# Kernel tuning notes

Measured on AMD Instinct MI355X. Metric: run time of the kernel, lower is better.

Reference implementation:

```python
import jax, jax.numpy as jnp
import numpy as np

STATE_DIM = 256
ACT_LEN = 16
LATENT = 256
ENC = 512
SLOPE = 0.01  # torch.nn.LeakyReLU() default


def _leaky(x):
    return jnp.where(x >= 0, x, SLOPE * x)


def setup_inputs() -> dict:
    key = jax.random.key(0)
    ks = jax.random.split(key, 16)
    B, T = 64, 1024
    D = STATE_DIM + 2 * ACT_LEN
    s = lambda k, shp, fan_in: jax.random.normal(k, shp, dtype=jnp.float32) * (1.0 / np.sqrt(fan_in))
    return {
        "padded_input": jax.random.normal(ks[0], (B, T, D), dtype=jnp.float32),
        # encoder: Linear(state,enc)+leaky, Linear(enc,enc)+leaky, Linear(enc,latent)+leaky
        "enc_w1": s(ks[1], (STATE_DIM, ENC), STATE_DIM), "enc_b1": jnp.zeros((ENC,), jnp.float32),
        "enc_w2": s(ks[2], (ENC, ENC), ENC),             "enc_b2": jnp.zeros((ENC,), jnp.float32),
        "enc_w3": s(ks[3], (ENC, LATENT), ENC),          "enc_b3": jnp.zeros((LATENT,), jnp.float32),
        # latent dynamics (bias-free)
        "A_w": s(ks[4], (LATENT, LATENT), LATENT),
        "B_w": s(ks[5], (ACT_LEN, LATENT), ACT_LEN),
        # decoder: Linear(latent,enc)+leaky, Linear(enc,enc)+leaky, Linear(enc,state)
        "dec_w1": s(ks[6], (LATENT, ENC), LATENT),       "dec_b1": jnp.zeros((ENC,), jnp.float32),
        "dec_w2": s(ks[7], (ENC, ENC), ENC),             "dec_b2": jnp.zeros((ENC,), jnp.float32),
        "dec_w3": s(ks[8], (ENC, STATE_DIM), ENC),       "dec_b3": jnp.zeros((STATE_DIM,), jnp.float32),
    }


def reference(padded_input, enc_w1, enc_b1, enc_w2, enc_b2, enc_w3, enc_b3,
              A_w, B_w, dec_w1, dec_b1, dec_w2, dec_b2, dec_w3, dec_b3):
    # slice features: [state | u_t | u_t1]
    x_t = padded_input[:, :, :STATE_DIM]                       # [B,T,S]
    u_t1 = padded_input[:, :, STATE_DIM + ACT_LEN:]            # [B,T,A]

    # encoder MLP
    h = _leaky(x_t @ enc_w1 + enc_b1)
    h = _leaky(h @ enc_w2 + enc_b2)
    z_t = _leaky(h @ enc_w3 + enc_b3)                          # [B,T,L]

    # reset_probability=0, nwarmup=0: t=0 uses z_t[:,0], then pure recurrence
    # z1[t] = A z1[t-1] + B u_t1[t]
    Bu = u_t1 @ B_w                                            # [B,T,L]

    def step(prev, bu_t):
        new = prev @ A_w + bu_t                                # [B,L]
        return new, new

    _, z1 = jax.lax.scan(step, z_t[:, 0, :], jnp.swapaxes(Bu, 0, 1))
    z_t1 = jnp.swapaxes(z1, 0, 1)                              # [B,T,L]

    # decoder MLP (last layer linear)
    h = _leaky(z_t1 @ dec_w1 + dec_b1)
    h = _leaky(h @ dec_w2 + dec_b2)
    x_t1 = h @ dec_w3 + dec_b3                                 # [B,T,S]
    return x_t1
```

## Files before the change

### kernel.cpp

```cpp
#include <hip/hip_runtime.h>

constexpr int Bb  = 64;
constexpr int Tt  = 1024;
constexpr int Dd  = 288;
constexpr int Ss  = 256;
constexpr int ALa = 16;
constexpr int Ll  = 256;
constexpr int Ee  = 512;
constexpr int CC  = 8;
constexpr int NCh = 128;
constexpr int NSC = 16;
constexpr int SC  = 8;
constexpr int DEC_CHUNKS = 8;
constexpr int DEC_ROWS = (Bb*Tt)/DEC_CHUNKS;

#define LKY(v) ((v) >= 0.f ? (v) : 0.01f*(v))

using f32x4  = __attribute__((ext_vector_type(4))) float;
using short8 = __attribute__((ext_vector_type(8))) short;
typedef unsigned short ushort_t;

__device__ __forceinline__ unsigned short f2bf(float f){
  unsigned int u = __float_as_uint(f);
  u = (u + 0x7fffu + ((u >> 16) & 1u)) >> 16;
  return (unsigned short)u;
}
__device__ __forceinline__ float bf2f(unsigned short h){
  return __uint_as_float(((unsigned int)h) << 16);
}

__global__ __launch_bounds__(256) void enc_fused(
    const float* __restrict__ in0,
    const float* __restrict__ w1, const float* __restrict__ b1,
    const float* __restrict__ w2, const float* __restrict__ b2,
    const float* __restrict__ w3, const float* __restrict__ b3,
    float* __restrict__ z0)
{
  int b = blockIdx.x, tid = threadIdx.x;
  __shared__ float xb[512], h1[512];
  xb[tid] = (tid < 256) ? in0[(long)b*(Tt*Dd) + tid] : 0.f;
  __syncthreads();
  float a0 = b1[tid], a1 = b1[tid+256];
  #pragma unroll 4
  for (int k = 0; k < 256; ++k){
    float xv = xb[k];
    a0 = fmaf(xv, w1[k*512 + tid      ], a0);
    a1 = fmaf(xv, w1[k*512 + tid + 256], a1);
  }
  __syncthreads();
  h1[tid] = LKY(a0); h1[tid+256] = LKY(a1);
  __syncthreads();
  float c0 = b2[tid], c1 = b2[tid+256];
  #pragma unroll 4
  for (int k = 0; k < 512; ++k){
    float hv = h1[k];
    c0 = fmaf(hv, w2[k*512 + tid      ], c0);
    c1 = fmaf(hv, w2[k*512 + tid + 256], c1);
  }
  __syncthreads();
  xb[tid] = LKY(c0); xb[tid+256] = LKY(c1);
  __syncthreads();
  float d0 = b3[tid];
  #pragma unroll 4
  for (int k = 0; k < 512; ++k)
    d0 = fmaf(xb[k], w3[k*256 + tid], d0);
  z0[b*256 + tid] = LKY(d0);
}

struct MMJob { const float* X; const float* Y; float* Cf; ushort_t* Ch; ushort_t* Cl; };
struct MMJobs { MMJob j[4]; };

__global__ __launch_bounds__(256) void matmul_gb(MMJobs jobs)
{
  MMJob jb = jobs.j[blockIdx.y];
  int i = blockIdx.x;
  int tid = threadIdx.x;
  int jg = tid & 63, tk = tid >> 6;
  __shared__ float row[256];
  __shared__ float4 part[4][64];
  if (tid < 256) row[tid] = jb.X[i*256 + tid];
  __syncthreads();
  int j4 = jg*4;
  float4 p0 = make_float4(0,0,0,0), p1 = make_float4(0,0,0,0);
  int kb = tk*64;
  #pragma unroll 4
  for (int k = kb; k < kb+64; k += 2){
    float x0 = row[k], x1 = row[k+1];
    float4 y0 = *(const float4*)&jb.Y[(k  )*256 + j4];
    float4 y1 = *(const float4*)&jb.Y[(k+1)*256 + j4];
    p0.x = fmaf(x0,y0.x,p0.x); p0.y = fmaf(x0,y0.y,p0.y);
    p0.z = fmaf(x0,y0.z,p0.z); p0.w = fmaf(x0,y0.w,p0.w);
    p1.x = fmaf(x1,y1.x,p1.x); p1.y = fmaf(x1,y1.y,p1.y);
    p1.z = fmaf(x1,y1.z,p1.z); p1.w = fmaf(x1,y1.w,p1.w);
  }
  p0.x+=p1.x; p0.y+=p1.y; p0.z+=p1.z; p0.w+=p1.w;
  part[tk][jg] = p0;
  __syncthreads();
  if (tid < 64){
    float4 s = part[0][tid];
    #pragma unroll
    for (int q = 1; q < 4; ++q){
      float4 v = part[q][tid];
      s.x+=v.x; s.y+=v.y; s.z+=v.z; s.w+=v.w;
    }
    int j = tid*4;
    if (jb.Cf) *(float4*)&jb.Cf[i*256 + j] = s;
    if (jb.Ch){
      float vv[4] = {s.x,s.y,s.z,s.w};
      #pragma unroll
      for (int e = 0; e < 4; ++e){
        ushort_t h = f2bf(vv[e]);
        int o = ((i>>3)*256 + j + e)*8 + (i&7);
        jb.Ch[o] = h; jb.Cl[o] = f2bf(vv[e] - bf2f(h));
      }
    }
  }
}

__global__ __launch_bounds__(256) void prep_a1bw(
    const float* __restrict__ A, const float* __restrict__ B,
    ushort_t* __restrict__ AH, ushort_t* __restrict__ AL,
    ushort_t* __restrict__ Bh, ushort_t* __restrict__ Bl)
{
  int o = blockIdx.x*256 + threadIdx.x;
  if (o < 65536){
    int j = o & 7, rest = o >> 3;
    int n = rest & 255, t8 = rest >> 8;
    int k = t8*8 + j;
    float v = A[k*256 + n];
    ushort_t h = f2bf(v);
    AH[o] = h; AL[o] = f2bf(v - bf2f(h));
  } else {
    int ob = o - 65536;
    int j = ob & 7, rest = ob >> 3;
    int n = rest & 255, kq = rest >> 8;
    int k = kq*8 + j;
    float v = (k < ALa) ? B[k*256 + n] : 0.f;
    ushort_t h = f2bf(v);
    Bh[ob] = h; Bl[ob] = f2bf(v - bf2f(h));
  }
}

__global__ __launch_bounds__(256) void prep_dec(
    const float* __restrict__ w1, const float* __restrict__ w2,
    const float* __restrict__ w3, ushort_t* __restrict__ Wh,
    ushort_t* __restrict__ Wl)
{
  long o = (long)blockIdx.x*256 + threadIdx.x;
  const float* W; ushort_t* H; ushort_t* L; int N; long oo;
  if (o < 131072){ W = w1; H = Wh;          L = Wl;          N = 512; oo = o; }
  else if (o < 393216){ W = w2; H = Wh + 131072; L = Wl + 131072; N = 512; oo = o - 131072; }
  else { W = w3; H = Wh + 393216; L = Wl + 393216; N = 256; oo = o - 393216; }
  int j = (int)(oo & 7);
  long rest = oo >> 3;
  int n = (int)(rest % N);
  int t8 = (int)(rest / N);
  int k = t8*8 + j;
  float v = W[(long)k*N + n];
  ushort_t h = f2bf(v);
  H[oo] = h; L[oo] = f2bf(v - bf2f(h));
}

__device__ __forceinline__ void load_afrag(
    const ushort_t* __restrict__ P, int kq, int m0, short8* dst)
{
  #pragma unroll
  for (int mt = 0; mt < 4; ++mt)
    dst[mt] = *(const short8*)&P[((long)kq*256 + m0 + mt*16)*8];
}

__global__ __launch_bounds__(256) void scan_mfma(
    const float* __restrict__ in0,
    const ushort_t* __restrict__ AtH, const ushort_t* __restrict__ AtL,
    const ushort_t* __restrict__ BtH, const ushort_t* __restrict__ BtL,
    float* __restrict__ wend, float* __restrict__ zout)
{
  int chunk = blockIdx.x;
  int n0 = blockIdx.y * 32;
  int tid = threadIdx.x;
  int wave = tid >> 6, lane = tid & 63;
  int quad = lane >> 4, l16 = lane & 15;
  int mwave = wave * 64;
  int m0 = mwave + l16;

  __shared__ ushort_t StH[8192];
  __shared__ ushort_t StL[8192];

  short8 Bfh[4], Bfl[4];
  #pragma unroll
  for (int mt = 0; mt < 4; ++mt){
    int off = ((quad)*256 + m0 + mt*16)*8;
    Bfh[mt] = *(const short8*)&BtH[off];
    Bfl[mt] = *(const short8*)&BtL[off];
  }

  f32x4 acc[4][2];
  #pragma unroll
  for (int mt = 0; mt < 4; ++mt)
    #pragma unroll
    for (int nt = 0; nt < 2; ++nt) acc[mt][nt] = (f32x4){0.f,0.f,0.f,0.f};

  const float* ubase[2];
  #pragma unroll
  for (int nt = 0; nt < 2; ++nt)
    ubase[nt] = in0 + (long)(n0 + nt*16 + l16)*(Tt*Dd) + (Ss + ALa) + quad*8;

  short8 Ahb[2][4], Alb[2][4];

  for (int tt = 0; tt < CC; ++tt){
    int t = chunk*CC + tt;
    float4 uq[2][2];
    #pragma unroll
    for (int nt = 0; nt < 2; ++nt){
      if (quad < 2){
        const float* up = ubase[nt] + (long)t*Dd;
        uq[nt][0] = *(const float4*)up;
        uq[nt][1] = *(const float4*)(up + 4);
      } else {
        uq[nt][0] = make_float4(0,0,0,0); uq[nt][1] = make_float4(0,0,0,0);
      }
    }

    if (tt > 0){
      load_afrag(AtH, 0*4 + quad, m0, Ahb[0]);
      load_afrag(AtL, 0*4 + quad, m0, Alb[0]);
      #pragma unroll
      for (int kt = 0; kt < 8; ++kt){
        int cur = kt & 1;
        if (kt < 7){
          load_afrag(AtH, (kt+1)*4 + quad, m0, Ahb[cur^1]);
          load_afrag(AtL, (kt+1)*4 + quad, m0, Alb[cur^1]);
        }
        short8 Sbh[2], Sbl[2];
        #pragma unroll
        for (int nt = 0; nt < 2; ++nt){
          int off = ((kt*4 + quad)*32 + nt*16 + l16)*8;
          Sbh[nt] = *(const short8*)&StH[off];
          Sbl[nt] = *(const short8*)&StL[off];
        }
        #pragma unroll
        for (int mt = 0; mt < 4; ++mt)
          #pragma unroll
          for (int nt = 0; nt < 2; ++nt){
            acc[mt][nt] = __builtin_amdgcn_mfma_f32_16x16x32_bf16(Ahb[cur][mt], Sbh[nt], acc[mt][nt], 0,0,0);
            acc[mt][nt] = __builtin_amdgcn_mfma_f32_16x16x32_bf16(Ahb[cur][mt], Sbl[nt], acc[mt][nt], 0,0,0);
            acc[mt][nt] = __builtin_amdgcn_mfma_f32_16x16x32_bf16(Alb[cur][mt], Sbh[nt], acc[mt][nt], 0,0,0);
          }
      }
    }

    short8 uh[2], ul[2];
    #pragma unroll
    for (int nt = 0; nt < 2; ++nt){
      float v[8] = {uq[nt][0].x,uq[nt][0].y,uq[nt][0].z,uq[nt][0].w,
                    uq[nt][1].x,uq[nt][1].y,uq[nt][1].z,uq[nt][1].w};
      ushort_t hs[8], ls[8];
      #pragma unroll
      for (int j = 0; j < 8; ++j){
        hs[j] = f2bf(v[j]);
        ls[j] = f2bf(v[j] - bf2f(hs[j]));
      }
      uh[nt] = *(const short8*)hs; ul[nt] = *(const short8*)ls;
    }
    #pragma unroll
    for (int mt = 0; mt < 4; ++mt)
      #pragma unroll
      for (int nt = 0; nt < 2; ++nt){
        acc[mt][nt] = __builtin_amdgcn_mfma_f32_16x16x32_bf16(Bfh[mt], uh[nt], acc[mt][nt], 0,0,0);
        acc[mt][nt] = __builtin_amdgcn_mfma_f32_16x16x32_bf16(Bfh[mt], ul[nt], acc[mt][nt], 0,0,0);
        acc[mt][nt] = __builtin_amdgcn_mfma_f32_16x16x32_bf16(Bfl[mt], uh[nt], acc[mt][nt], 0,0,0);
      }

    __syncthreads();

    #pragma unroll
    for (int mt = 0; mt < 4; ++mt){
      int mb = mwave + mt*16 + quad*4;
      #pragma unroll
      for (int nt = 0; nt < 2; ++nt){
        int n = nt*16 + l16;
        int gn = n0 + n;
        f32x4 v = acc[mt][nt];
        *(float4*)&zout[((long)gn*Tt + t)*Ll + mb] = make_float4(v[0],v[1],v[2],v[3]);
        if (tt == CC-1)
          *(float4*)&wend[((long)chunk*Bb + gn)*Ll + mb] = make_float4(v[0],v[1],v[2],v[3]);
        #pragma unroll
        for (int reg = 0; reg < 4; ++reg){
          int m = mb + reg;
          ushort_t h = f2bf(v[reg]);
          ushort_t l = f2bf(v[reg] - bf2f(h));
          int so = ((m>>3)*32 + n)*8 + (m&7);
          StH[so] = h; StL[so] = l;
        }
        acc[mt][nt] = (f32x4){0.f,0.f,0.f,0.f};
      }
    }
    __syncthreads();
  }
}

__device__ __forceinline__ void frag_init_state512(
    const float* __restrict__ src, ushort_t* StH, ushort_t* StL, int tid)
{
  #pragma unroll
  for (int it = 0; it < 4; ++it){
    int idx = tid + it*512;
    int m8 = idx >> 6, n = idx & 63;
    const float* p = src + (long)n*256 + m8*8;
    float4 v0 = *(const float4*)p;
    float4 v1 = *(const float4*)(p + 4);
    float vv[8] = {v0.x,v0.y,v0.z,v0.w,v1.x,v1.y,v1.z,v1.w};
    ushort_t hs[8], ls[8];
    #pragma unroll
    for (int j = 0; j < 8; ++j){
      hs[j] = f2bf(vv[j]);
      ls[j] = f2bf(vv[j] - bf2f(hs[j]));
    }
    *(uint4*)&StH[(m8*64 + n)*8] = *(const uint4*)hs;
    *(uint4*)&StL[(m8*64 + n)*8] = *(const uint4*)ls;
  }
}

__device__ __forceinline__ void p2_load_A(
    const ushort_t* __restrict__ PH, const ushort_t* __restrict__ PL,
    int wave, int lane, short8 Ah[2][8], short8 Al[2][8])
{
  int quad = lane >> 4, l16 = lane & 15;
  int m0 = wave*32 + l16;
  #pragma unroll
  for (int kt = 0; kt < 8; ++kt){
    int kq = kt*4 + quad;
    #pragma unroll
    for (int mt = 0; mt < 2; ++mt){
      Ah[mt][kt] = *(const short8*)&PH[((long)kq*256 + m0 + mt*16)*8];
      Al[mt][kt] = *(const short8*)&PL[((long)kq*256 + m0 + mt*16)*8];
    }
  }
}

__device__ __forceinline__ void ks_gemm_body(
    const ushort_t* __restrict__ PH, const ushort_t* __restrict__ PL,
    const float* __restrict__ accsrc, const float* __restrict__ bsrc,
    float* __restrict__ outp, ushort_t* StH, ushort_t* StL)
{
  int tid = threadIdx.x;
  int wave = tid >> 6, lane = tid & 63;
  int quad = lane >> 4, l16 = lane & 15;
  int mwave = wave*32;

  short8 Ah[2][8], Al[2][8];
  p2_load_A(PH, PL, wave, lane, Ah, Al);
  frag_init_state512(bsrc, StH, StL, tid);

  f32x4 acc[2][4];
  #pragma unroll
  for (int mt = 0; mt < 2; ++mt){
    int mb = mwave + mt*16 + quad*4;
    #pragma unroll
    for (int nt = 0; nt < 4; ++nt){
      int n = nt*16 + l16;
      float4 v = *(const float4*)&accsrc[(long)n*256 + mb];
      acc[mt][nt] = (f32x4){v.x, v.y, v.z, v.w};
    }
  }
  __syncthreads();

  #pragma unroll
  for (int kt = 0; kt < 8; ++kt){
    #pragma unroll
    for (int nt = 0; nt < 4; ++nt){
      int off = ((kt*4 + quad)*64 + nt*16 + l16)*8;
      short8 Sbh = *(const short8*)&StH[off];
      short8 Sbl = *(const short8*)&StL[off];
      #pragma unroll
      for (int mt = 0; mt < 2; ++mt){
        acc[mt][nt] = __builtin_amdgcn_mfma_f32_16x16x32_bf16(Ah[mt][kt], Sbh, acc[mt][nt], 0,0,0);
        acc[mt][nt] = __builtin_amdgcn_mfma_f32_16x16x32_bf16(Ah[mt][kt], Sbl, acc[mt][nt], 0,0,0);
        acc[mt][nt] = __builtin_amdgcn_mfma_f32_16x16x32_bf16(Al[mt][kt], Sbh, acc[mt][nt], 0,0,0);
      }
    }
  }

  #pragma unroll
  for (int mt = 0; mt < 2; ++mt){
    int mb = mwave + mt*16 + quad*4;
    #pragma unroll
    for (int nt = 0; nt < 4; ++nt){
      int n = nt*16 + l16;
      f32x4 v = acc[mt][nt];
      *(float4*)&outp[(long)n*256 + mb] = make_float4(v[0],v[1],v[2],v[3]);
    }
  }
}

__device__ __forceinline__ const float* ks_src(
    const float* __restrict__ in, const float* __restrict__ z0,
    const float* __restrict__ pbend, int c, int init_mode)
{
  if (!init_mode) return in + (long)c*(Bb*Ll);
  return (c == 0) ? z0 : (pbend + (long)(8*c - 1)*(Bb*Ll));
}

__global__ __launch_bounds__(512) void ks_round(
    const ushort_t* __restrict__ PH, const ushort_t* __restrict__ PL,
    const float* __restrict__ in, const float* __restrict__ z0,
    const float* __restrict__ pbend,
    float* __restrict__ out, long outStride, int d, int local_seg, int init_mode)
{
  int c = blockIdx.x;
  int tid = threadIdx.x;
  int pos = local_seg ? (c & 7) : c;
  const float* src_c = ks_src(in, z0, pbend, c, init_mode);
  float* op = out + (long)c*outStride;

  if (pos < d){
    const float4* s4p = (const float4*)src_c;
    float4* d4p = (float4*)op;
    #pragma unroll
    for (int it = 0; it < 8; ++it) d4p[tid + it*512] = s4p[tid + it*512];
    return;
  }
  const float* src_cd = ks_src(in, z0, pbend, c - d, init_mode);
  __shared__ ushort_t StH[16384], StL[16384];
  ks_gemm_body(PH, PL, src_c, src_cd, op, StH, StL);
}

__global__ __launch_bounds__(512) void replay_corr(
    const ushort_t* __restrict__ A8H, const ushort_t* __restrict__ A8L,
    const ushort_t* __restrict__ A8PH, const ushort_t* __restrict__ A8PL,
    const float* __restrict__ pb, float* __restrict__ inits)
{
  int i = blockIdx.x + 1;
  int s = blockIdx.y;
  const ushort_t* PH = (i == 1) ? A8H : (A8PH + (long)(i-1)*65536);
  const ushort_t* PL = (i == 1) ? A8L : (A8PL + (long)(i-1)*65536);
  __shared__ ushort_t StH[16384], StL[16384];
  ks_gemm_body(PH, PL,
               pb + (long)(8*s + i - 1)*(Bb*Ll),
               inits + (long)(8*s)*(Bb*Ll),
               inits + (long)(8*s + i)*(Bb*Ll), StH, StL);
}

__global__ __launch_bounds__(256) void gemm_corr(
    const float* __restrict__ inits, const ushort_t* __restrict__ AjH,
    const ushort_t* __restrict__ AjL, float* __restrict__ out)
{
  int jz = blockIdx.z;
  const ushort_t* Whp = AjH + (long)jz*65536;
  const ushort_t* Wlp = AjL + (long)jz*65536;
  __shared__ __align__(16) ushort_t Xh[4*128*8], Xl[4*128*8];
  __shared__ __align__(16) ushort_t Wh[4*128*8], Wl[4*128*8];

  int tid  = threadIdx.x;
  int wave = tid >> 6, lane = tid & 63;
  int wm = wave & 1, wn = wave >> 1;
  int quad = lane >> 4, l16 = lane & 15;
  int row0 = blockIdx.y * 128;
  int col0 = blockIdx.x * 128;

  f32x4 acc[4][4];
  #pragma unroll
  for (int mt = 0; mt < 4; ++mt)
    #pragma unroll
    for (int nt = 0; nt < 4; ++nt) acc[mt][nt] = (f32x4){0.f,0.f,0.f,0.f};

  for (int kt = 0; kt < 8; ++kt){
    #pragma unroll
    for (int it = 0; it < 2; ++it){
      int idx = tid + it*256;
      int q = idx >> 7, m = idx & 127;
      const float* xp = &inits[(long)(row0 + m)*256 + kt*32 + q*8];
      float4 v0 = *(const float4*)xp;
      float4 v1 = *(const float4*)(xp + 4);
      float vv[8] = {v0.x,v0.y,v0.z,v0.w,v1.x,v1.y,v1.z,v1.w};
      ushort_t hs[8], ls[8];
      #pragma unroll
      for (int j = 0; j < 8; ++j){
        hs[j] = f2bf(vv[j]);
        ls[j] = f2bf(vv[j] - bf2f(hs[j]));
      }
      *(uint4*)&Xh[(q*128 + m)*8] = *(const uint4*)hs;
      *(uint4*)&Xl[(q*128 + m)*8] = *(const uint4*)ls;
      int n = idx & 127;
      long src = (long)(kt*4 + q)*256 + col0 + n;
      ((uint4*)Wh)[q*128 + n] = ((const uint4*)Whp)[src];
      ((uint4*)Wl)[q*128 + n] = ((const uint4*)Wlp)[src];
    }
    __syncthreads();
    short8 ah[4], al[4], bh[4], bl[4];
    #pragma unroll
    for (int mt = 0; mt < 4; ++mt){
      int off = (quad*128 + wm*64 + mt*16 + l16)*8;
      ah[mt] = *(const short8*)&Xh[off];
      al[mt] = *(const short8*)&Xl[off];
    }
    #pragma unroll
    for (int nt = 0; nt < 4; ++nt){
      int off = (quad*128 + wn*64 + nt*16 + l16)*8;
      bh[nt] = *(const short8*)&Wh[off];
      bl[nt] = *(const short8*)&Wl[off];
    }
    #pragma unroll
    for (int mt = 0; mt < 4; ++mt)
      #pragma unroll
      for (int nt = 0; nt < 4; ++nt){
        acc[mt][nt] = __builtin_amdgcn_mfma_f32_16x16x32_bf16(ah[mt], bh[nt], acc[mt][nt], 0,0,0);
        acc[mt][nt] = __builtin_amdgcn_mfma_f32_16x16x32_bf16(ah[mt], bl[nt], acc[mt][nt], 0,0,0);
        acc[mt][nt] = __builtin_amdgcn_mfma_f32_16x16x32_bf16(al[mt], bh[nt], acc[mt][nt], 0,0,0);
      }
    __syncthreads();
  }

  #pragma unroll
  for (int mt = 0; mt < 4; ++mt){
    #pragma unroll
    for (int nt = 0; nt < 4; ++nt){
      int col = col0 + wn*64 + nt*16 + l16;
      #pragma unroll
      for (int reg = 0; reg < 4; ++reg){
        int row = row0 + wm*64 + mt*16 + quad*4 + reg;
        int b = row & 63, c = row >> 6;
        int t = c*CC + jz;
        long addr = ((long)b*Tt + t)*Ll + col;
        out[addr] += acc[mt][nt][reg];
      }
    }
  }
}

template<int BM, int BN, bool INS, bool OUTS>
__global__ __launch_bounds__(256) void gemm_mfma(
    const float* __restrict__ X,
    const ushort_t* __restrict__ Xhp, const ushort_t* __restrict__ Xlp,
    const ushort_t* __restrict__ Whp, const ushort_t* __restrict__ Wlp,
    const float* __restrict__ bias, float* __restrict__ Y,
    ushort_t* __restrict__ Yh, ushort_t* __restrict__ Yl,
    int Mrows, int K, int N, int act)
{
  constexpr int BMh = BM/2, BNh = BN/2;
  constexpr int MT = BM/32, NT = BN/32;
  __shared__ __align__(16) ushort_t Xh[4*BM*8], Xl[4*BM*8];
  __shared__ __align__(16) ushort_t Wh[4*BN*8], Wl[4*BN*8];

  int tid  = threadIdx.x;
  int wave = tid >> 6, lane = tid & 63;
  int wm = wave & 1, wn = wave >> 1;
  int quad = lane >> 4, l16 = lane & 15;
  long row0 = (long)blockIdx.y * BM;
  int col0 = blockIdx.x * BN;

  f32x4 acc[MT][NT];
  #pragma unroll
  for (int mt = 0; mt < MT; ++mt)
    #pragma unroll
    for (int nt = 0; nt < NT; ++nt) acc[mt][nt] = (f32x4){0.f,0.f,0.f,0.f};

  for (int kt = 0; kt < K; kt += 32){
    int ktile = kt >> 5;
    if constexpr (INS){
      #pragma unroll
      for (int it = 0; it < (BM*4)/256; ++it){
        int idx = tid + it*256;
        int q = idx / BM, m = idx % BM;
        long src = (long)(ktile*4 + q)*Mrows + row0 + m;
        ((uint4*)Xh)[q*BM + m] = ((const uint4*)Xhp)[src];
        ((uint4*)Xl)[q*BM + m] = ((const uint4*)Xlp)[src];
      }
    } else {
      #pragma unroll
      for (int it = 0; it < (BM*4)/256; ++it){
        int idx = tid + it*256;
        int q = idx / BM, m = idx % BM;
        const float* xp = &X[(row0 + m)*(long)K + kt + q*8];
        float4 v0 = *(const float4*)xp;
        float4 v1 = *(const float4*)(xp + 4);
        float vv[8] = {v0.x,v0.y,v0.z,v0.w,v1.x,v1.y,v1.z,v1.w};
        ushort_t hs[8], ls[8];
        #pragma unroll
        for (int j = 0; j < 8; ++j){
          hs[j] = f2bf(vv[j]);
          ls[j] = f2bf(vv[j] - bf2f(hs[j]));
        }
        *(uint4*)&Xh[(q*BM + m)*8] = *(const uint4*)hs;
        *(uint4*)&Xl[(q*BM + m)*8] = *(const uint4*)ls;
      }
    }
    #pragma unroll
    for (int it = 0; it < (BN*4)/256; ++it){
      int idx = tid + it*256;
      int q = idx / BN, n = idx % BN;
      long src = (long)(ktile*4 + q)*N + col0 + n;
      ((uint4*)Wh)[q*BN + n] = ((const uint4*)Whp)[src];
      ((uint4*)Wl)[q*BN + n] = ((const uint4*)Wlp)[src];
    }
    __syncthreads();

    short8 ah[MT], al[MT], bh[NT], bl[NT];
    #pragma unroll
    for (int mt = 0; mt < MT; ++mt){
      int off = (quad*BM + wm*BMh + mt*16 + l16)*8;
      ah[mt] = *(const short8*)&Xh[off];
      al[mt] = *(const short8*)&Xl[off];
    }
    #pragma unroll
    for (int nt = 0; nt < NT; ++nt){
      int off = (quad*BN + wn*BNh + nt*16 + l16)*8;
      bh[nt] = *(const short8*)&Wh[off];
      bl[nt] = *(const short8*)&Wl[off];
    }
    #pragma unroll
    for (int mt = 0; mt < MT; ++mt)
      #pragma unroll
      for (int nt = 0; nt < NT; ++nt){
        acc[mt][nt] = __builtin_amdgcn_mfma_f32_16x16x32_bf16(ah[mt], bh[nt], acc[mt][nt], 0, 0, 0);
        acc[mt][nt] = __builtin_amdgcn_mfma_f32_16x16x32_bf16(ah[mt], bl[nt], acc[mt][nt], 0, 0, 0);
        acc[mt][nt] = __builtin_amdgcn_mfma_f32_16x16x32_bf16(al[mt], bh[nt], acc[mt][nt], 0, 0, 0);
      }
    __syncthreads();
  }

  #pragma unroll
  for (int mt = 0; mt < MT; ++mt){
    long rowb = row0 + wm*BMh + mt*16 + quad*4;
    #pragma unroll
    for (int nt = 0; nt < NT; ++nt){
      int col = col0 + wn*BNh + nt*16 + l16;
      float bs = bias[col];
      #pragma unroll
      for (int reg = 0; reg < 4; ++reg){
        float y = acc[mt][nt][reg] + bs;
        if (act) y = LKY(y);
        long row = rowb + reg;
        if constexpr (OUTS){
          ushort_t h = f2bf(y);
          ushort_t l = f2bf(y - bf2f(h));
          long off = ((long)(col >> 3)*Mrows + row)*8 + (col & 7);
          Yh[off] = h; Yl[off] = l;
        } else {
          Y[row*(long)N + col] = y;
        }
      }
    }
  }
}

extern "C" void kernel_launch(void* const* d_in, const int* in_sizes, int n_in,
                              void* d_out, int out_size, void* d_ws, size_t ws_size,
                              hipStream_t stream) {
  const float* in0    = (const float*)d_in[0];
  const float* enc_w1 = (const float*)d_in[1];
  const float* enc_b1 = (const float*)d_in[2];
  const float* enc_w2 = (const float*)d_in[3];
  const float* enc_b2 = (const float*)d_in[4];
  const float* enc_w3 = (const float*)d_in[5];
  const float* enc_b3 = (const float*)d_in[6];
  const float* A_w    = (const float*)d_in[7];
  const float* B_w    = (const float*)d_in[8];
  const float* dec_w1 = (const float*)d_in[9];
  const float* dec_b1 = (const float*)d_in[10];
  const float* dec_w2 = (const float*)d_in[11];
  const float* dec_b2 = (const float*)d_in[12];
  const float* dec_w3 = (const float*)d_in[13];
  const float* dec_b3 = (const float*)d_in[14];
  float* out = (float*)d_out;

  float* ws    = (float*)d_ws;
  float* s2    = ws + 65536;
  float* s3    = ws + 131072;
  float* s4    = ws + 196608;
  float* s8    = ws + 262144;
  float* s16   = ws + 327680;
  float* s32   = ws + 393216;
  float* s64   = ws + 458752;
  ushort_t* Whp_d = (ushort_t*)(ws + 524288);
  ushort_t* Wlp_d = (ushort_t*)(ws + 786432);
  float* Rf    = ws + 1048576;
  ushort_t* AjH = (ushort_t*)Rf;
  ushort_t* AjL = (ushort_t*)(Rf + 262144);
  ushort_t* BtH = (ushort_t*)(Rf + 524288);
  ushort_t* BtL = BtH + 8192;
  float* wend  = Rf + 532480;
  float* inits = Rf + 2629632;
  float* g0    = Rf + 4726784;
  ushort_t* A64H = (ushort_t*)(Rf + 4988928);
  ushort_t* A64L = (ushort_t*)(Rf + 5021696);
  float* pb0   = Rf + 5054464;
  ushort_t* A8PH = (ushort_t*)(Rf + 7151616);
  ushort_t* A8PL = (ushort_t*)(Rf + 7380992);
  ushort_t* A64PH = (ushort_t*)(Rf + 7610368);
  ushort_t* A64PL = (ushort_t*)(Rf + 7708672);
  float* f24   = Rf + 7806976;
  float* f128  = Rf + 7872512;
  float* f256  = Rf + 7938048;
  float* g1    = Rf + 8003584;
  ushort_t* h1h = (ushort_t*)Rf;
  ushort_t* h1l = (ushort_t*)(Rf + 2097152);
  ushort_t* h2h = (ushort_t*)(Rf + 4194304);
  ushort_t* h2l = (ushort_t*)(Rf + 6291456);
  ushort_t* A8H = AjH + 7*65536;
  ushort_t* A8L = AjL + 7*65536;

  enc_fused<<<64, 256, 0, stream>>>(in0, enc_w1, enc_b1, enc_w2, enc_b2,
                                    enc_w3, enc_b3, inits);

  prep_a1bw<<<288, 256, 0, stream>>>(A_w, B_w, AjH, AjL, BtH, BtL);

  auto mj = [](const float* X, const float* Y, float* Cf, ushort_t* Ch, ushort_t* Cl){
    MMJob r; r.X = X; r.Y = Y; r.Cf = Cf; r.Ch = Ch; r.Cl = Cl; return r;
  };
  { MMJobs J = {};
    J.j[0] = mj(A_w, A_w, s2, AjH+1*65536, AjL+1*65536);
    matmul_gb<<<dim3(256,1), 256, 0, stream>>>(J); }
  { MMJobs J = {};
    J.j[0] = mj(s2, A_w, s3, AjH+2*65536, AjL+2*65536);
    J.j[1] = mj(s2, s2,  s4, AjH+3*65536, AjL+3*65536);
    matmul_gb<<<dim3(256,2), 256, 0, stream>>>(J); }
  { MMJobs J = {};
    J.j[0] = mj(s4, A_w, nullptr, AjH+4*65536, AjL+4*65536);
    J.j[1] = mj(s4, s2,  nullptr, AjH+5*65536, AjL+5*65536);
    J.j[2] = mj(s4, s3,  nullptr, AjH+6*65536, AjL+6*65536);
    J.j[3] = mj(s4, s4,  s8, A8H, A8L);
    matmul_gb<<<dim3(256,4), 256, 0, stream>>>(J); }
  { MMJobs J = {};
    J.j[0] = mj(s8, s8, s16, A8PH+1*65536, A8PL+1*65536);
    matmul_gb<<<dim3(256,1), 256, 0, stream>>>(J); }
  { MMJobs J = {};
    J.j[0] = mj(s16, s8,  f24, A8PH+2*65536, A8PL+2*65536);
    J.j[1] = mj(s16, s16, s32, A8PH+3*65536, A8PL+3*65536);
    matmul_gb<<<dim3(256,2), 256, 0, stream>>>(J); }
  { MMJobs J = {};
    J.j[0] = mj(s32, s8,  nullptr, A8PH+4*65536, A8PL+4*65536);
    J.j[1] = mj(s32, s16, nullptr, A8PH+5*65536, A8PL+5*65536);
    J.j[2] = mj(s32, f24, nullptr, A8PH+6*65536, A8PL+6*65536);
    J.j[3] = mj(s32, s32, s64, A64H, A64L);
    matmul_gb<<<dim3(256,4), 256, 0, stream>>>(J); }
  { MMJobs J = {};
    J.j[0] = mj(s64, s64, f128, A64PH+0*65536, A64PL+0*65536);
    matmul_gb<<<dim3(256,1), 256, 0, stream>>>(J); }
  { MMJobs J = {};
    J.j[0] = mj(f128, f128, f256, A64PH+1*65536, A64PL+1*65536);
    matmul_gb<<<dim3(256,1), 256, 0, stream>>>(J); }
  { MMJobs J = {};
    J.j[0] = mj(f256, f256, nullptr, A64PH+2*65536, A64PL+2*65536);
    matmul_gb<<<dim3(256,1), 256, 0, stream>>>(J); }

  prep_dec<<<2048, 256, 0, stream>>>(dec_w1, dec_w2, dec_w3, Whp_d, Wlp_d);

  scan_mfma<<<dim3(NCh, 2), 256, 0, stream>>>(in0, AjH, AjL, BtH, BtL, wend, out);

  ks_round<<<128, 512, 0, stream>>>(A8H, A8L, wend, nullptr, nullptr, pb0, Bb*Ll, 1, 1, 0);
  ks_round<<<128, 512, 0, stream>>>(A8PH+1*65536, A8PL+1*65536, pb0, nullptr, nullptr, wend, Bb*Ll, 2, 1, 0);
  ks_round<<<128, 512, 0, stream>>>(A8PH+3*65536, A8PL+3*65536, wend, nullptr, nullptr, pb0, Bb*Ll, 4, 1, 0);
  ks_round<<<16, 512, 0, stream>>>(A64H, A64L, nullptr, inits, pb0, g1, Bb*Ll, 1, 0, 1);
  ks_round<<<16, 512, 0, stream>>>(A64PH+0*65536, A64PL+0*65536, g1, nullptr, nullptr, g0, Bb*Ll, 2, 0, 0);
  ks_round<<<16, 512, 0, stream>>>(A64PH+1*65536, A64PL+1*65536, g0, nullptr, nullptr, g1, Bb*Ll, 4, 0, 0);
  ks_round<<<16, 512, 0, stream>>>(A64PH+2*65536, A64PL+2*65536, g1, nullptr, nullptr, inits, (long)SC*Bb*Ll, 8, 0, 0);
  replay_corr<<<dim3(7, 16), 512, 0, stream>>>(A8H, A8L, A8PH, A8PL, pb0, inits);

  gemm_corr<<<dim3(2, 64, 8), 256, 0, stream>>>(inits, AjH, AjL, out);

  for (int rc = 0; rc < DEC_CHUNKS; ++rc){
    const float* zc = out + (long)rc*DEC_ROWS*Ll;
    float* oc       = out + (long)rc*DEC_ROWS*Ll;
    gemm_mfma<64,128,false,true><<<dim3(Ee/128, DEC_ROWS/64), 256, 0, stream>>>(
        zc, nullptr, nullptr, Whp_d, Wlp_d, dec_b1, nullptr, h1h, h1l, DEC_ROWS, Ll, Ee, 1);
    gemm_mfma<64,128,true,true><<<dim3(Ee/128, DEC_ROWS/64), 256, 0, stream>>>(
        nullptr, h1h, h1l, Whp_d + 131072, Wlp_d + 131072, dec_b2, nullptr, h2h, h2l, DEC_ROWS, Ee, Ee, 1);
    gemm_mfma<64,128,true,false><<<dim3(Ss/128, DEC_ROWS/64), 256, 0, stream>>>(
        nullptr, h2h, h2l, Whp_d + 393216, Wlp_d + 393216, dec_b3, oc, nullptr, nullptr, DEC_ROWS, Ee, Ss, 0);
  }
}
```

Before: 1.021 ms.

## Split encoder into parallel dense layer kernels and enlarge decoder GEMM tiles

The single-block-per-batch fused encoder, which ran only 64 blocks, is replaced by three launches of a generic dense kernel. Each launch is split over output-column tiles with a K-split shared-memory reduction, so many more blocks run in parallel. Intermediate activations now go through workspace memory, which adds launches and global traffic. Separately, the first two decoder GEMMs use 128-row tiles instead of 64, which halves the grid size and raises weight reuse per block.

```diff
diff --git a/kernel.cpp b/kernel.cpp
--- a/kernel.cpp
+++ b/kernel.cpp
@@ -29,42 +29,38 @@
   return __uint_as_float(((unsigned int)h) << 16);
 }
 
-__global__ __launch_bounds__(256) void enc_fused(
-    const float* __restrict__ in0,
-    const float* __restrict__ w1, const float* __restrict__ b1,
-    const float* __restrict__ w2, const float* __restrict__ b2,
-    const float* __restrict__ w3, const float* __restrict__ b3,
-    float* __restrict__ z0)
-{
-  int b = blockIdx.x, tid = threadIdx.x;
-  __shared__ float xb[512], h1[512];
-  xb[tid] = (tid < 256) ? in0[(long)b*(Tt*Dd) + tid] : 0.f;
+__global__ __launch_bounds__(256) void enc_dense(
+    const float* __restrict__ xin, int xstride,
+    const float* __restrict__ W, const float* __restrict__ bias,
+    float* __restrict__ out, int K, int N, int act)
+{
+  int b = blockIdx.x, col0 = blockIdx.y * 32;
+  int tid = threadIdx.x;
+  int tx = tid & 31, tk = tid >> 5;
+  __shared__ float x[512];
+  __shared__ float part[8][33];
+  for (int k = tid; k < K; k += 256) x[k] = xin[(long)b*xstride + k];
   __syncthreads();
-  float a0 = b1[tid], a1 = b1[tid+256];
-  #pragma unroll 4
-  for (int k = 0; k < 256; ++k){
-    float xv = xb[k];
-    a0 = fmaf(xv, w1[k*512 + tid      ], a0);
-    a1 = fmaf(xv, w1[k*512 + tid + 256], a1);
-  }
+  int j = col0 + tx;
+  float p0=0.f,p1=0.f,p2=0.f,p3=0.f;
+  int iters = K >> 3;
+  #pragma unroll 2
+  for (int i = 0; i < iters; i += 4){
+    int k0 = tk + 8*i;
+    p0 = fmaf(x[k0     ], W[(long)(k0     )*N + j], p0);
+    p1 = fmaf(x[k0 +  8], W[(long)(k0 +  8)*N + j], p1);
+    p2 = fmaf(x[k0 + 16], W[(long)(k0 + 16)*N + j], p2);
+    p3 = fmaf(x[k0 + 24], W[(long)(k0 + 24)*N + j], p3);
+  }
+  part[tk][tx] = (p0+p1)+(p2+p3);
   __syncthreads();
-  h1[tid] = LKY(a0); h1[tid+256] = LKY(a1);
-  __syncthreads();
-  float c0 = b2[tid], c1 = b2[tid+256];
-  #pragma unroll 4
-  for (int k = 0; k < 512; ++k){
-    float hv = h1[k];
-    c0 = fmaf(hv, w2[k*512 + tid      ], c0);
-    c1 = fmaf(hv, w2[k*512 + tid + 256], c1);
-  }
-  __syncthreads();
-  xb[tid] = LKY(c0); xb[tid+256] = LKY(c1);
-  __syncthreads();
-  float d0 = b3[tid];
-  #pragma unroll 4
-  for (int k = 0; k < 512; ++k)
-    d0 = fmaf(xb[k], w3[k*256 + tid], d0);
-  z0[b*256 + tid] = LKY(d0);
+  if (tid < 32){
+    float s = part[0][tid];
+    #pragma unroll
+    for (int q = 1; q < 8; ++q) s += part[q][tid];
+    s += bias[col0 + tid];
+    out[b*N + col0 + tid] = act ? LKY(s) : s;
+  }
 }
 
 struct MMJob { const float* X; const float* Y; float* Cf; ushort_t* Ch; ushort_t* Cl; };
@@ -665,6 +661,8 @@
   float* out = (float*)d_out;
 
   float* ws    = (float*)d_ws;
+  float* h1enc = ws;
+  float* h2enc = ws + 32768;
   float* s2    = ws + 65536;
   float* s3    = ws + 131072;
   float* s4    = ws + 196608;
@@ -700,8 +698,9 @@
   ushort_t* A8H = AjH + 7*65536;
   ushort_t* A8L = AjL + 7*65536;
 
-  enc_fused<<<64, 256, 0, stream>>>(in0, enc_w1, enc_b1, enc_w2, enc_b2,
-                                    enc_w3, enc_b3, inits);
+  enc_dense<<<dim3(64,16), 256, 0, stream>>>(in0, Tt*Dd, enc_w1, enc_b1, h1enc, 256, 512, 1);
+  enc_dense<<<dim3(64,16), 256, 0, stream>>>(h1enc, 512, enc_w2, enc_b2, h2enc, 512, 512, 1);
+  enc_dense<<<dim3(64, 8), 256, 0, stream>>>(h2enc, 512, enc_w3, enc_b3, inits, 512, 256, 1);
 
   prep_a1bw<<<288, 256, 0, stream>>>(A_w, B_w, AjH, AjL, BtH, BtL);
 
@@ -762,9 +761,9 @@
   for (int rc = 0; rc < DEC_CHUNKS; ++rc){
     const float* zc = out + (long)rc*DEC_ROWS*Ll;
     float* oc       = out + (long)rc*DEC_ROWS*Ll;
-    gemm_mfma<64,128,false,true><<<dim3(Ee/128, DEC_ROWS/64), 256, 0, stream>>>(
+    gemm_mfma<128,128,false,true><<<dim3(Ee/128, DEC_ROWS/128), 256, 0, stream>>>(
         zc, nullptr, nullptr, Whp_d, Wlp_d, dec_b1, nullptr, h1h, h1l, DEC_ROWS, Ll, Ee, 1);
-    gemm_mfma<64,128,true,true><<<dim3(Ee/128, DEC_ROWS/64), 256, 0, stream>>>(
+    gemm_mfma<128,128,true,true><<<dim3(Ee/128, DEC_ROWS/128), 256, 0, stream>>>(
         nullptr, h1h, h1l, Whp_d + 131072, Wlp_d + 131072, dec_b2, nullptr, h2h, h2l, DEC_ROWS, Ee, Ee, 1);
     gemm_mfma<64,128,true,false><<<dim3(Ss/128, DEC_ROWS/64), 256, 0, stream>>>(
         nullptr, h2h, h2l, Whp_d + 393216, Wlp_d + 393216, dec_b3, oc, nullptr, nullptr, DEC_ROWS, Ee, Ss, 0);
```

Result: no change. 1.032 ms (+1.0%).
